# Kernel tuning notes

Hardware: AMD Instinct MI355X
Metric: run time of the kernel (lower is better)

The kernel has to match this reference:

```python
import jax, jax.numpy as jnp
import numpy as np
import math

B, N, E, H = 2, 10000, 160000, 128
ET = 8
EPS = 1e-5


def setup_inputs() -> dict:
    key = jax.random.key(0)
    ks = jax.random.split(key, 20)
    s = 1.0 / math.sqrt(H)
    inp = {
        "hidden": jax.random.normal(ks[0], (B, N, H), jnp.float32),
        "time_emb": jax.random.normal(ks[1], (B, N, H), jnp.float32),
        "edge_index": jax.random.randint(ks[2], (2, E), 0, N),
        "edge_type": jax.random.randint(ks[3], (E,), 0, ET),
        # parameters
        "edge_emb": jax.random.normal(ks[4], (ET, H), jnp.float32),
        "Wq": jax.random.normal(ks[5], (H, H), jnp.float32) * s,
        "bq": jnp.zeros((H,), jnp.float32),
        "Wk": jax.random.normal(ks[6], (H, H), jnp.float32) * s,
        "bk": jnp.zeros((H,), jnp.float32),
        "Wv": jax.random.normal(ks[7], (H, H), jnp.float32) * s,
        "bv": jnp.zeros((H,), jnp.float32),
        "We": jax.random.normal(ks[8], (H, 1), jnp.float32) * s,
        "be": jnp.zeros((1,), jnp.float32),
        "W1": jax.random.normal(ks[9], (3 * H, H), jnp.float32) * (1.0 / math.sqrt(3 * H)),
        "b1": jnp.zeros((H,), jnp.float32),
        "W2": jax.random.normal(ks[10], (H, H), jnp.float32) * s,
        "b2": jnp.zeros((H,), jnp.float32),
        "gamma": jnp.ones((H,), jnp.float32),
        "beta": jnp.zeros((H,), jnp.float32),
    }
    return inp


def _forward(hidden, time_emb, edge_index, edge_type, edge_emb,
             Wq, bq, Wk, bk, Wv, bv, We, be, W1, b1, W2, b2, gamma, beta):
    src, tgt = edge_index[0], edge_index[1]
    # edge-wise gathers: [B, E, H]
    src_h = hidden[:, src]
    tgt_h = hidden[:, tgt]
    src_t = time_emb[:, src]
    tgt_t = time_emb[:, tgt]
    edge_h = edge_emb[edge_type][None, :, :]  # [1, E, H] broadcasts over batch

    query = (tgt_h + tgt_t) @ Wq + bq
    key = (src_h + src_t + edge_h) @ Wk + bk
    value = (src_h + edge_h) @ Wv + bv

    logits = jnp.einsum("beh,beh->be", query, key) / math.sqrt(H)
    logits = logits + (edge_h @ We + be)[..., 0]  # edge bias broadcast over batch

    # segment softmax per target node (equivalent to the per-node masked softmax loop)
    lT = logits.T  # [E, B]
    seg_max = jax.ops.segment_max(lT, tgt, num_segments=N)          # [N, B]
    seg_max = jnp.where(jnp.isfinite(seg_max), seg_max, 0.0)
    ex = jnp.exp(lT - seg_max[tgt])                                  # [E, B]
    seg_sum = jax.ops.segment_sum(ex, tgt, num_segments=N)           # [N, B]
    weights = (ex / seg_sum[tgt]).T                                  # [B, E]

    messages = value * weights[..., None]                            # [B, E, H]
    # scatter-add to target nodes
    agg = jax.ops.segment_sum(jnp.swapaxes(messages, 0, 1), tgt, num_segments=N)  # [N, B, H]
    aggregated = jnp.swapaxes(agg, 0, 1)                             # [B, N, H]

    cat = jnp.concatenate([hidden, aggregated, time_emb], axis=-1)   # [B, N, 3H]
    updated = jax.nn.silu(cat @ W1 + b1) @ W2 + b2

    x = hidden + updated  # dropout p=0 -> identity
    mu = jnp.mean(x, axis=-1, keepdims=True)
    var = jnp.var(x, axis=-1, keepdims=True)
    return (x - mu) * jax.lax.rsqrt(var + EPS) * gamma + beta


def reference(hidden, time_emb, edge_index, edge_type, edge_emb,
              Wq, bq, Wk, bk, Wv, bv, We, be, W1, b1, W2, b2, gamma, beta):
    return _forward(hidden, time_emb, edge_index, edge_type, edge_emb,
                    Wq, bq, Wk, bk, Wv, bv, We, be, W1, b1, W2, b2, gamma, beta)
```

## Files before the change

kernel.cpp:

```cpp
#include <hip/hip_runtime.h>
#include <math.h>

constexpr int B_  = 2;
constexpr int N_  = 10000;
constexpr int E_  = 160000;
constexpr int H_  = 128;
constexpr int ET_ = 8;
constexpr float EPS_ = 1e-5f;
constexpr float RSQH = 0.08838834764831845f;

typedef __bf16 bf16x8 __attribute__((ext_vector_type(8)));
typedef short  short8 __attribute__((ext_vector_type(8)));
typedef float  f32x4  __attribute__((ext_vector_type(4)));
typedef unsigned short u16;

__device__ inline u16 bf16b(float f) {
    return __builtin_bit_cast(u16, (__bf16)f);
}

__device__ inline bf16x8 ldfrag(const u16* __restrict__ W, int kc, int nt, int lane) {
    short8 s = *(const short8*)(W + ((kc * 8 + nt) * 64 + lane) * 8);
    return __builtin_bit_cast(bf16x8, s);
}

__global__ __launch_bounds__(256)
void setup_kernel(const float* __restrict__ W1, const float* __restrict__ W2,
                  const float* __restrict__ Wq, const float* __restrict__ Wk,
                  const float* __restrict__ Wv,
                  u16* __restrict__ W1s, u16* __restrict__ W2s,
                  u16* __restrict__ Wqs, u16* __restrict__ Wks, u16* __restrict__ Wvs,
                  const float* __restrict__ edge_emb,
                  const float* __restrict__ bk, const float* __restrict__ bv,
                  const float* __restrict__ We, const float* __restrict__ be,
                  float* __restrict__ Kt, float* __restrict__ Vt, float* __restrict__ eb,
                  const int* __restrict__ tgt, int* __restrict__ hist)
{
    const int bid = blockIdx.x, tid = threadIdx.x;
    if (bid < 56) {
        int unit = bid >> 1, half = bid & 1;
        const float* src; u16* dst; int kc;
        if (unit < 12)      { src = W1; dst = W1s; kc = unit; }
        else if (unit < 16) { src = W2; dst = W2s; kc = unit - 12; }
        else if (unit < 20) { src = Wq; dst = Wqs; kc = unit - 16; }
        else if (unit < 24) { src = Wk; dst = Wks; kc = unit - 20; }
        else                { src = Wv; dst = Wvs; kc = unit - 24; }
        int nt = half * 4 + (tid >> 6), lane = tid & 63;
        int q = lane >> 4, c = lane & 15;
        int kbase = kc * 32 + q * 8;
        int col = nt * 16 + c;
        u16* out = dst + ((kc * 8 + nt) * 64 + lane) * 8;
#pragma unroll
        for (int j = 0; j < 8; ++j)
            out[j] = bf16b(src[(kbase + j) * H_ + col]);
    } else if (bid < 64) {
        int t = bid - 56;
        const float* ep = edge_emb + t * H_;
        __shared__ float red[2];
        int j = tid;
        if (j < 128) {
            float ak = bk[j], av = bv[j];
            for (int d = 0; d < H_; d += 4) {
                float e0 = ep[d], e1 = ep[d+1], e2 = ep[d+2], e3 = ep[d+3];
                ak += e0*Wk[(d+0)*H_+j] + e1*Wk[(d+1)*H_+j] + e2*Wk[(d+2)*H_+j] + e3*Wk[(d+3)*H_+j];
                av += e0*Wv[(d+0)*H_+j] + e1*Wv[(d+1)*H_+j] + e2*Wv[(d+2)*H_+j] + e3*Wv[(d+3)*H_+j];
            }
            Kt[t*H_ + j] = ak;
            Vt[t*H_ + j] = av;
            float pe = ep[j] * We[j];
#pragma unroll
            for (int off = 32; off; off >>= 1) pe += __shfl_xor(pe, off);
            if ((j & 63) == 0) red[j >> 6] = pe;
        }
        __syncthreads();
        if (j == 0) eb[t] = red[0] + red[1] + be[0];
    } else {
        int e = (bid - 64) * 256 + tid;
        if (e < E_) atomicAdd(&hist[tgt[e]], 1);
    }
}

__global__ __launch_bounds__(1024)
void scan_kernel(const int* __restrict__ hist, int* __restrict__ offs,
                 int* __restrict__ cursor)
{
    __shared__ int winc[16];
    const int tid = threadIdx.x, wave = tid >> 6, lane = tid & 63;
    int v[10];
    const int idx0 = tid * 10;
    int tot = 0;
#pragma unroll
    for (int i = 0; i < 10; ++i) {
        int idx = idx0 + i;
        v[i] = (idx < N_) ? hist[idx] : 0;
        tot += v[i];
    }
    int s = tot;
#pragma unroll
    for (int off = 1; off < 64; off <<= 1) {
        int t = __shfl_up(s, off);
        if (lane >= off) s += t;
    }
    if (lane == 63) winc[wave] = s;
    __syncthreads();
    if (tid < 16) {
        int si = winc[tid];
#pragma unroll
        for (int off = 1; off < 16; off <<= 1) {
            int t = __shfl_up(si, off);
            if (tid >= off) si += t;
        }
        winc[tid] = si;
    }
    __syncthreads();
    int wbase = (wave == 0) ? 0 : winc[wave - 1];
    int run = wbase + (s - tot);
#pragma unroll
    for (int i = 0; i < 10; ++i) {
        int idx = idx0 + i;
        if (idx < N_) { offs[idx] = run; cursor[idx] = run; }
        run += v[i];
    }
    if (tid == 0) offs[N_] = winc[15];
}

__global__ __launch_bounds__(256)
void scatter_qkv_kernel(const int* __restrict__ src, const int* __restrict__ tgt,
                        const int* __restrict__ type, int* __restrict__ cursor,
                        int* __restrict__ sorted,
                        const float* __restrict__ hidden, const float* __restrict__ time_emb,
                        const u16* __restrict__ Wqs, const u16* __restrict__ Wks,
                        const u16* __restrict__ Wvs, const float* __restrict__ bq,
                        u16* __restrict__ Q, u16* __restrict__ K, u16* __restrict__ V)
{
    if (blockIdx.x < 625) {
        int e = blockIdx.x * 256 + threadIdx.x;
        if (e < E_) {
            int t = tgt[e];
            int pos = atomicAdd(&cursor[t], 1);
            sorted[pos] = src[e] | (type[e] << 16);
        }
        return;
    }
    const int wv = threadIdx.x >> 6, lane = threadIdx.x & 63;
    const int tile = (blockIdx.x - 625) * 4 + wv;
    if (tile >= (B_ * N_) / 16) return;
    const int nbase = tile * 16;
    const int m = lane & 15, q = lane >> 4;
    const int koff = q * 8;

    bf16x8 aq[4], av[4];
    const float* hp = hidden   + (nbase + m) * H_ + koff;
    const float* tp = time_emb + (nbase + m) * H_ + koff;
#pragma unroll
    for (int kc = 0; kc < 4; ++kc) {
        float4 h0 = *(const float4*)(hp + kc * 32);
        float4 h1 = *(const float4*)(hp + kc * 32 + 4);
        float4 t0 = *(const float4*)(tp + kc * 32);
        float4 t1 = *(const float4*)(tp + kc * 32 + 4);
        bf16x8 fv, fq;
        fv[0]=(__bf16)h0.x; fv[1]=(__bf16)h0.y; fv[2]=(__bf16)h0.z; fv[3]=(__bf16)h0.w;
        fv[4]=(__bf16)h1.x; fv[5]=(__bf16)h1.y; fv[6]=(__bf16)h1.z; fv[7]=(__bf16)h1.w;
        fq[0]=(__bf16)(h0.x+t0.x); fq[1]=(__bf16)(h0.y+t0.y);
        fq[2]=(__bf16)(h0.z+t0.z); fq[3]=(__bf16)(h0.w+t0.w);
        fq[4]=(__bf16)(h1.x+t1.x); fq[5]=(__bf16)(h1.y+t1.y);
        fq[6]=(__bf16)(h1.z+t1.z); fq[7]=(__bf16)(h1.w+t1.w);
        av[kc] = fv; aq[kc] = fq;
    }

    f32x4 accq[8], acck[8], accv[8];
#pragma unroll
    for (int nt = 0; nt < 8; ++nt) { accq[nt] = (f32x4)0.f; acck[nt] = (f32x4)0.f; accv[nt] = (f32x4)0.f; }

#pragma unroll
    for (int kc = 0; kc < 4; ++kc) {
#pragma unroll
        for (int nt = 0; nt < 8; ++nt) {
            bf16x8 bfq = ldfrag(Wqs, kc, nt, lane);
            bf16x8 bfk = ldfrag(Wks, kc, nt, lane);
            bf16x8 bfv = ldfrag(Wvs, kc, nt, lane);
            accq[nt] = __builtin_amdgcn_mfma_f32_16x16x32_bf16(aq[kc], bfq, accq[nt], 0, 0, 0);
            acck[nt] = __builtin_amdgcn_mfma_f32_16x16x32_bf16(aq[kc], bfk, acck[nt], 0, 0, 0);
            accv[nt] = __builtin_amdgcn_mfma_f32_16x16x32_bf16(av[kc], bfv, accv[nt], 0, 0, 0);
        }
    }

#pragma unroll
    for (int nt = 0; nt < 8; ++nt) {
        int col = nt * 16 + m;
        float bqc = bq[col];
#pragma unroll
        for (int r = 0; r < 4; ++r) {
            int node = nbase + q * 4 + r;
            Q[node * H_ + col] = bf16b(accq[nt][r] + bqc);
            K[node * H_ + col] = bf16b(acck[nt][r]);
            V[node * H_ + col] = bf16b(accv[nt][r]);
        }
    }
}

__global__ __launch_bounds__(256)
void attn_kernel(const u16* __restrict__ Qb, const u16* __restrict__ Kb,
                 const u16* __restrict__ Vb,
                 const float* __restrict__ Kt, const float* __restrict__ Vt,
                 const float* __restrict__ eb,
                 const int* __restrict__ offs, const int* __restrict__ sorted,
                 u16* __restrict__ aggb)
{
    __shared__ float logit_s[4][64];
    __shared__ float bias_s[4][8];
    __shared__ int   pk_s[4][64];
    __shared__ __align__(16) u16 vt_s[8][128];

    const int tid = threadIdx.x;
    const int wv = tid >> 6, lane = tid & 63;
    const int g = lane >> 4, lam = lane & 15;

    for (int idx = tid; idx < ET_ * H_; idx += 256)
        vt_s[idx >> 7][idx & 127] = bf16b(Vt[idx]);
    __syncthreads();

    const int b = blockIdx.x & 1;
    const int n = (blockIdx.x >> 1) * 4 + wv;
    const int bn = b * N_ + n;
    const int beg = offs[n], end = offs[n + 1];
    const int bbase = b * N_;

    float q[8];
    {
        short8 s8 = *(const short8*)(Qb + (size_t)bn * H_ + lam * 8);
        bf16x8 qa = __builtin_bit_cast(bf16x8, s8);
#pragma unroll
        for (int j = 0; j < 8; ++j) q[j] = (float)qa[j];
    }

    {
        const float* k0p = Kt + (2 * g) * H_ + lam * 8;
        const float* k1p = Kt + (2 * g + 1) * H_ + lam * 8;
        float p0 = 0.f, p1 = 0.f;
#pragma unroll
        for (int j = 0; j < 8; ++j) { p0 += q[j] * k0p[j]; p1 += q[j] * k1p[j]; }
#pragma unroll
        for (int msk = 1; msk < 16; msk <<= 1) {
            p0 += __shfl_xor(p0, msk);
            p1 += __shfl_xor(p1, msk);
        }
        if (lam == 0) {
            bias_s[wv][2 * g]     = p0 * RSQH + eb[2 * g];
            bias_s[wv][2 * g + 1] = p1 * RSQH + eb[2 * g + 1];
        }
    }

    float m_run = -INFINITY, l = 0.f;
    float acc[8];
#pragma unroll
    for (int j = 0; j < 8; ++j) acc[j] = 0.f;

    for (int cb = beg; cb < end; cb += 64) {
        const int cnt = min(64, end - cb);
        pk_s[wv][lane] = (cb + lane < end) ? sorted[cb + lane] : 0;

        float gmax = -INFINITY;
        int c = g;
        for (; c + 4 < cnt; c += 8) {
            int pk0 = pk_s[wv][c];
            int pk1 = pk_s[wv][c + 4];
            int s0 = pk0 & 0xFFFF, t0 = pk0 >> 16;
            int s1 = pk1 & 0xFFFF, t1 = pk1 >> 16;
            short8 k80 = *(const short8*)(Kb + (size_t)(bbase + s0) * H_ + lam * 8);
            short8 k81 = *(const short8*)(Kb + (size_t)(bbase + s1) * H_ + lam * 8);
            bf16x8 ka0 = __builtin_bit_cast(bf16x8, k80);
            bf16x8 ka1 = __builtin_bit_cast(bf16x8, k81);
            float p0 = 0.f, p1 = 0.f;
#pragma unroll
            for (int j = 0; j < 8; ++j) {
                p0 += q[j] * (float)ka0[j];
                p1 += q[j] * (float)ka1[j];
            }
#pragma unroll
            for (int msk = 1; msk < 16; msk <<= 1) {
                p0 += __shfl_xor(p0, msk);
                p1 += __shfl_xor(p1, msk);
            }
            float lg0 = p0 * RSQH + bias_s[wv][t0];
            float lg1 = p1 * RSQH + bias_s[wv][t1];
            if (lam == 0) { logit_s[wv][c] = lg0; logit_s[wv][c + 4] = lg1; }
            gmax = fmaxf(gmax, fmaxf(lg0, lg1));
        }
        if (c < cnt) {
            int pk0 = pk_s[wv][c];
            int s0 = pk0 & 0xFFFF, t0 = pk0 >> 16;
            short8 k80 = *(const short8*)(Kb + (size_t)(bbase + s0) * H_ + lam * 8);
            bf16x8 ka0 = __builtin_bit_cast(bf16x8, k80);
            float p0 = 0.f;
#pragma unroll
            for (int j = 0; j < 8; ++j) p0 += q[j] * (float)ka0[j];
#pragma unroll
            for (int msk = 1; msk < 16; msk <<= 1) p0 += __shfl_xor(p0, msk);
            float lg0 = p0 * RSQH + bias_s[wv][t0];
            if (lam == 0) logit_s[wv][c] = lg0;
            gmax = fmaxf(gmax, lg0);
        }
        gmax = fmaxf(gmax, __shfl_xor(gmax, 16));
        gmax = fmaxf(gmax, __shfl_xor(gmax, 32));
        float Mn = fmaxf(m_run, gmax);
        float rs = __expf(m_run - Mn);
        l *= rs;
#pragma unroll
        for (int j = 0; j < 8; ++j) acc[j] *= rs;
        m_run = Mn;

        c = g;
        for (; c + 4 < cnt; c += 8) {
            int pk0 = pk_s[wv][c];
            int pk1 = pk_s[wv][c + 4];
            int s0 = pk0 & 0xFFFF, t0 = pk0 >> 16;
            int s1 = pk1 & 0xFFFF, t1 = pk1 >> 16;
            short8 v80  = *(const short8*)(Vb + (size_t)(bbase + s0) * H_ + lam * 8);
            short8 v81  = *(const short8*)(Vb + (size_t)(bbase + s1) * H_ + lam * 8);
            short8 vt80 = *(const short8*)(&vt_s[t0][lam * 8]);
            short8 vt81 = *(const short8*)(&vt_s[t1][lam * 8]);
            float w0 = __expf(logit_s[wv][c] - Mn);
            float w1 = __expf(logit_s[wv][c + 4] - Mn);
            l += w0 + w1;
            bf16x8 va0  = __builtin_bit_cast(bf16x8, v80);
            bf16x8 va1  = __builtin_bit_cast(bf16x8, v81);
            bf16x8 vta0 = __builtin_bit_cast(bf16x8, vt80);
            bf16x8 vta1 = __builtin_bit_cast(bf16x8, vt81);
#pragma unroll
            for (int j = 0; j < 8; ++j)
                acc[j] += w0 * ((float)va0[j] + (float)vta0[j])
                        + w1 * ((float)va1[j] + (float)vta1[j]);
        }
        if (c < cnt) {
            int pk0 = pk_s[wv][c];
            int s0 = pk0 & 0xFFFF, t0 = pk0 >> 16;
            short8 v80  = *(const short8*)(Vb + (size_t)(bbase + s0) * H_ + lam * 8);
            short8 vt80 = *(const short8*)(&vt_s[t0][lam * 8]);
            float w0 = __expf(logit_s[wv][c] - Mn);
            l += w0;
            bf16x8 va0  = __builtin_bit_cast(bf16x8, v80);
            bf16x8 vta0 = __builtin_bit_cast(bf16x8, vt80);
#pragma unroll
            for (int j = 0; j < 8; ++j)
                acc[j] += w0 * ((float)va0[j] + (float)vta0[j]);
        }
    }

#pragma unroll
    for (int j = 0; j < 8; ++j) {
        acc[j] += __shfl_xor(acc[j], 16);
        acc[j] += __shfl_xor(acc[j], 32);
    }
    l += __shfl_xor(l, 16);
    l += __shfl_xor(l, 32);

    if (g == 0) {
        float invL = (end > beg) ? 1.f / l : 0.f;
        bf16x8 o;
#pragma unroll
        for (int j = 0; j < 8; ++j) o[j] = (__bf16)(acc[j] * invL);
        *(short8*)(aggb + (size_t)bn * H_ + lam * 8) = __builtin_bit_cast(short8, o);
    }
}

__global__ __launch_bounds__(256)
void mlp_mfma_kernel(const float* __restrict__ hidden, const u16* __restrict__ aggb,
                     const float* __restrict__ time_emb,
                     const u16* __restrict__ W1s, const u16* __restrict__ W2s,
                     const float* __restrict__ b1, const float* __restrict__ b2,
                     const float* __restrict__ gamma, const float* __restrict__ beta,
                     float* __restrict__ out)
{
    __shared__ __align__(16) u16 h1s[4][16][136];
    const int wv = threadIdx.x >> 6, lane = threadIdx.x & 63;
    const int tile = blockIdx.x * 4 + wv;
    if (tile >= (B_ * N_) / 16) return;
    const int nbase = tile * 16;
    const int m = lane & 15, q = lane >> 4;
    const int koff = q * 8;

    bf16x8 a[12];
    const float* hp = hidden   + (nbase + m) * H_ + koff;
    const float* tp = time_emb + (nbase + m) * H_ + koff;
    const u16*   ap = aggb + (size_t)(nbase + m) * H_ + koff;
#pragma unroll
    for (int kc = 0; kc < 4; ++kc) {
        float4 h0 = *(const float4*)(hp + kc * 32);
        float4 h1 = *(const float4*)(hp + kc * 32 + 4);
        float4 t0 = *(const float4*)(tp + kc * 32);
        float4 t1 = *(const float4*)(tp + kc * 32 + 4);
        bf16x8 fh, ft;
        fh[0]=(__bf16)h0.x; fh[1]=(__bf16)h0.y; fh[2]=(__bf16)h0.z; fh[3]=(__bf16)h0.w;
        fh[4]=(__bf16)h1.x; fh[5]=(__bf16)h1.y; fh[6]=(__bf16)h1.z; fh[7]=(__bf16)h1.w;
        ft[0]=(__bf16)t0.x; ft[1]=(__bf16)t0.y; ft[2]=(__bf16)t0.z; ft[3]=(__bf16)t0.w;
        ft[4]=(__bf16)t1.x; ft[5]=(__bf16)t1.y; ft[6]=(__bf16)t1.z; ft[7]=(__bf16)t1.w;
        a[0 * 4 + kc] = fh;
        a[2 * 4 + kc] = ft;
        short8 s8 = *(const short8*)(ap + kc * 32);
        a[1 * 4 + kc] = __builtin_bit_cast(bf16x8, s8);
    }

    f32x4 acc[8];
#pragma unroll
    for (int nt = 0; nt < 8; ++nt) acc[nt] = (f32x4)0.f;
#pragma unroll
    for (int kc = 0; kc < 12; ++kc) {
#pragma unroll
        for (int nt = 0; nt < 8; ++nt) {
            bf16x8 bf = ldfrag(W1s, kc, nt, lane);
            acc[nt] = __builtin_amdgcn_mfma_f32_16x16x32_bf16(a[kc], bf, acc[nt], 0, 0, 0);
        }
    }

#pragma unroll
    for (int nt = 0; nt < 8; ++nt) {
        int col = nt * 16 + m;
        float bb = b1[col];
#pragma unroll
        for (int r = 0; r < 4; ++r) {
            float v = acc[nt][r] + bb;
            float h = v / (1.f + __expf(-v));
            h1s[wv][q * 4 + r][col] = bf16b(h);
        }
    }

    f32x4 acc2[8];
#pragma unroll
    for (int nt = 0; nt < 8; ++nt) acc2[nt] = (f32x4)0.f;
#pragma unroll
    for (int kc = 0; kc < 4; ++kc) {
        short8 s8 = *(const short8*)&h1s[wv][m][kc * 32 + koff];
        bf16x8 a2 = __builtin_bit_cast(bf16x8, s8);
#pragma unroll
        for (int nt = 0; nt < 8; ++nt) {
            bf16x8 bf = ldfrag(W2s, kc, nt, lane);
            acc2[nt] = __builtin_amdgcn_mfma_f32_16x16x32_bf16(a2, bf, acc2[nt], 0, 0, 0);
        }
    }

    float x[8][4];
#pragma unroll
    for (int nt = 0; nt < 8; ++nt) {
        int col = nt * 16 + m;
        float bb = b2[col];
#pragma unroll
        for (int r = 0; r < 4; ++r) {
            int node = nbase + q * 4 + r;
            x[nt][r] = hidden[node * H_ + col] + acc2[nt][r] + bb;
        }
    }
#pragma unroll
    for (int r = 0; r < 4; ++r) {
        float s = 0.f, ss = 0.f;
#pragma unroll
        for (int nt = 0; nt < 8; ++nt) { s += x[nt][r]; ss += x[nt][r] * x[nt][r]; }
#pragma unroll
        for (int off = 1; off < 16; off <<= 1) {
            s  += __shfl_xor(s, off);
            ss += __shfl_xor(ss, off);
        }
        float mu  = s * (1.f / H_);
        float var = ss * (1.f / H_) - mu * mu;
        float rs  = rsqrtf(var + EPS_);
        int node = nbase + q * 4 + r;
#pragma unroll
        for (int nt = 0; nt < 8; ++nt) {
            int col = nt * 16 + m;
            out[node * H_ + col] = (x[nt][r] - mu) * rs * gamma[col] + beta[col];
        }
    }
}

extern "C" void kernel_launch(void* const* d_in, const int* in_sizes, int n_in,
                              void* d_out, int out_size, void* d_ws, size_t ws_size,
                              hipStream_t stream)
{
    const float* hidden   = (const float*)d_in[0];
    const float* time_emb = (const float*)d_in[1];
    const int*   eidx     = (const int*)d_in[2];
    const int*   etype    = (const int*)d_in[3];
    const float* edge_emb = (const float*)d_in[4];
    const float* Wq = (const float*)d_in[5];
    const float* bq = (const float*)d_in[6];
    const float* Wk = (const float*)d_in[7];
    const float* bk = (const float*)d_in[8];
    const float* Wv = (const float*)d_in[9];
    const float* bv = (const float*)d_in[10];
    const float* We = (const float*)d_in[11];
    const float* be = (const float*)d_in[12];
    const float* W1 = (const float*)d_in[13];
    const float* b1 = (const float*)d_in[14];
    const float* W2 = (const float*)d_in[15];
    const float* b2 = (const float*)d_in[16];
    const float* gamma = (const float*)d_in[17];
    const float* beta  = (const float*)d_in[18];
    float* out = (float*)d_out;

    constexpr int BNH = B_ * N_ * H_;
    u16* Qb   = (u16*)d_ws;
    u16* Kb   = Qb + BNH;
    u16* Vb   = Kb + BNH;
    u16* aggb = Vb + BNH;
    float* Kt  = (float*)(aggb + BNH);
    float* Vt  = Kt + ET_ * H_;
    float* ebt = Vt + ET_ * H_;
    int* hist   = (int*)(ebt + ET_);
    int* offs   = hist + N_;
    int* cursor = offs + (N_ + 1);
    int* sorted = cursor + N_;
    uintptr_t wp = (uintptr_t)(sorted + E_);
    wp = (wp + 15) & ~(uintptr_t)15;
    u16* W1s = (u16*)wp;
    u16* W2s = W1s + 384 * 128;
    u16* Wqs = W2s + 128 * 128;
    u16* Wks = Wqs + 128 * 128;
    u16* Wvs = Wks + 128 * 128;

    const int* esrc = eidx;
    const int* etgt = eidx + E_;

    hipMemsetAsync(hist, 0, N_ * sizeof(int), stream);

    setup_kernel<<<64 + (E_ + 255) / 256, 256, 0, stream>>>(
        W1, W2, Wq, Wk, Wv, W1s, W2s, Wqs, Wks, Wvs,
        edge_emb, bk, bv, We, be, Kt, Vt, ebt, etgt, hist);
    scan_kernel<<<1, 1024, 0, stream>>>(hist, offs, cursor);
    scatter_qkv_kernel<<<625 + 313, 256, 0, stream>>>(
        esrc, etgt, etype, cursor, sorted,
        hidden, time_emb, Wqs, Wks, Wvs, bq, Qb, Kb, Vb);
    attn_kernel<<<(B_ * N_) / 4, 256, 0, stream>>>(Qb, Kb, Vb, Kt, Vt, ebt, offs, sorted, aggb);
    mlp_mfma_kernel<<<313, 256, 0, stream>>>(hidden, aggb, time_emb, W1s, W2s, b1, b2, gamma, beta, out);
}
```

Before: 195.7 us.

## Single-pass per-group online softmax in attention; precompute edge-type bias in QKV kernel

The attention kernel drops its two-pass chunk structure (logits to shared memory, then a max, then a second pass over V) in favour of one pass. Each 16-lane group keeps its own running max and sum, and K and V loads are issued together. Groups are merged with shuffles at the end. The per-node edge-type bias (q·Kt) moves into the QKV projection kernel, computed from fp32 accumulators and stored as a B*N*8 table. This removes a shared-memory round trip and a second gather loop, at the cost of extra exp and rescale work per edge and more register pressure.

```diff
diff --git a/kernel.cpp b/kernel.cpp
--- a/kernel.cpp
+++ b/kernel.cpp
@@ -130,7 +130,9 @@
                         const float* __restrict__ hidden, const float* __restrict__ time_emb,
                         const u16* __restrict__ Wqs, const u16* __restrict__ Wks,
                         const u16* __restrict__ Wvs, const float* __restrict__ bq,
-                        u16* __restrict__ Q, u16* __restrict__ K, u16* __restrict__ V)
+                        const float* __restrict__ KtF, const float* __restrict__ ebt,
+                        u16* __restrict__ Q, u16* __restrict__ K, u16* __restrict__ V,
+                        float* __restrict__ biasT)
 {
     if (blockIdx.x < 625) {
         int e = blockIdx.x * 256 + threadIdx.x;
@@ -184,14 +186,35 @@
         }
     }
 
+    float bqv[8];
+#pragma unroll
+    for (int nt = 0; nt < 8; ++nt) bqv[nt] = bq[nt * 16 + m];
+
+#pragma unroll
+    for (int t = 0; t < ET_; ++t) {
+        float kt[8];
+#pragma unroll
+        for (int nt = 0; nt < 8; ++nt) kt[nt] = KtF[t * H_ + nt * 16 + m];
+        float ebv = ebt[t];
+#pragma unroll
+        for (int r = 0; r < 4; ++r) {
+            float s = 0.f;
+#pragma unroll
+            for (int nt = 0; nt < 8; ++nt) s += (accq[nt][r] + bqv[nt]) * kt[nt];
+#pragma unroll
+            for (int msk = 1; msk < 16; msk <<= 1) s += __shfl_xor(s, msk);
+            if (m == 0)
+                biasT[(nbase + q * 4 + r) * ET_ + t] = s * RSQH + ebv;
+        }
+    }
+
 #pragma unroll
     for (int nt = 0; nt < 8; ++nt) {
         int col = nt * 16 + m;
-        float bqc = bq[col];
 #pragma unroll
         for (int r = 0; r < 4; ++r) {
             int node = nbase + q * 4 + r;
-            Q[node * H_ + col] = bf16b(accq[nt][r] + bqc);
+            Q[node * H_ + col] = bf16b(accq[nt][r] + bqv[nt]);
             K[node * H_ + col] = bf16b(acck[nt][r]);
             V[node * H_ + col] = bf16b(accv[nt][r]);
         }
@@ -200,20 +223,18 @@
 
 __global__ __launch_bounds__(256)
 void attn_kernel(const u16* __restrict__ Qb, const u16* __restrict__ Kb,
-                 const u16* __restrict__ Vb,
-                 const float* __restrict__ Kt, const float* __restrict__ Vt,
-                 const float* __restrict__ eb,
+                 const u16* __restrict__ Vb, const float* __restrict__ Vt,
+                 const float* __restrict__ biasT,
                  const int* __restrict__ offs, const int* __restrict__ sorted,
                  u16* __restrict__ aggb)
 {
-    __shared__ float logit_s[4][64];
     __shared__ float bias_s[4][8];
     __shared__ int   pk_s[4][64];
     __shared__ __align__(16) u16 vt_s[8][128];
 
     const int tid = threadIdx.x;
     const int wv = tid >> 6, lane = tid & 63;
-    const int g = lane >> 4, lam = lane & 15;
+    const int g = lane >> 4, lam = lane & 63 & 15;
 
     for (int idx = tid; idx < ET_ * H_; idx += 256)
         vt_s[idx >> 7][idx & 127] = bf16b(Vt[idx]);
@@ -225,6 +246,8 @@
     const int beg = offs[n], end = offs[n + 1];
     const int bbase = b * N_;
 
+    if (lane < 8) bias_s[wv][lane] = biasT[bn * ET_ + lane];
+
     float q[8];
     {
         short8 s8 = *(const short8*)(Qb + (size_t)bn * H_ + lam * 8);
@@ -233,24 +256,7 @@
         for (int j = 0; j < 8; ++j) q[j] = (float)qa[j];
     }
 
-    {
-        const float* k0p = Kt + (2 * g) * H_ + lam * 8;
-        const float* k1p = Kt + (2 * g + 1) * H_ + lam * 8;
-        float p0 = 0.f, p1 = 0.f;
-#pragma unroll
-        for (int j = 0; j < 8; ++j) { p0 += q[j] * k0p[j]; p1 += q[j] * k1p[j]; }
-#pragma unroll
-        for (int msk = 1; msk < 16; msk <<= 1) {
-            p0 += __shfl_xor(p0, msk);
-            p1 += __shfl_xor(p1, msk);
-        }
-        if (lam == 0) {
-            bias_s[wv][2 * g]     = p0 * RSQH + eb[2 * g];
-            bias_s[wv][2 * g + 1] = p1 * RSQH + eb[2 * g + 1];
-        }
-    }
-
-    float m_run = -INFINITY, l = 0.f;
+    float m_g = -INFINITY, l_g = 0.f;
     float acc[8];
 #pragma unroll
     for (int j = 0; j < 8; ++j) acc[j] = 0.f;
@@ -259,7 +265,6 @@
         const int cnt = min(64, end - cb);
         pk_s[wv][lane] = (cb + lane < end) ? sorted[cb + lane] : 0;
 
-        float gmax = -INFINITY;
         int c = g;
         for (; c + 4 < cnt; c += 8) {
             int pk0 = pk_s[wv][c];
@@ -268,6 +273,10 @@
             int s1 = pk1 & 0xFFFF, t1 = pk1 >> 16;
             short8 k80 = *(const short8*)(Kb + (size_t)(bbase + s0) * H_ + lam * 8);
             short8 k81 = *(const short8*)(Kb + (size_t)(bbase + s1) * H_ + lam * 8);
+            short8 v80 = *(const short8*)(Vb + (size_t)(bbase + s0) * H_ + lam * 8);
+            short8 v81 = *(const short8*)(Vb + (size_t)(bbase + s1) * H_ + lam * 8);
+            short8 vt80 = *(const short8*)(&vt_s[t0][lam * 8]);
+            short8 vt81 = *(const short8*)(&vt_s[t1][lam * 8]);
             bf16x8 ka0 = __builtin_bit_cast(bf16x8, k80);
             bf16x8 ka1 = __builtin_bit_cast(bf16x8, k81);
             float p0 = 0.f, p1 = 0.f;
@@ -283,13 +292,27 @@
             }
             float lg0 = p0 * RSQH + bias_s[wv][t0];
             float lg1 = p1 * RSQH + bias_s[wv][t1];
-            if (lam == 0) { logit_s[wv][c] = lg0; logit_s[wv][c + 4] = lg1; }
-            gmax = fmaxf(gmax, fmaxf(lg0, lg1));
+            float nm = fmaxf(m_g, fmaxf(lg0, lg1));
+            float sc = __expf(m_g - nm);
+            float w0 = __expf(lg0 - nm);
+            float w1 = __expf(lg1 - nm);
+            l_g = l_g * sc + w0 + w1;
+            bf16x8 va0  = __builtin_bit_cast(bf16x8, v80);
+            bf16x8 va1  = __builtin_bit_cast(bf16x8, v81);
+            bf16x8 vta0 = __builtin_bit_cast(bf16x8, vt80);
+            bf16x8 vta1 = __builtin_bit_cast(bf16x8, vt81);
+#pragma unroll
+            for (int j = 0; j < 8; ++j)
+                acc[j] = acc[j] * sc + w0 * ((float)va0[j] + (float)vta0[j])
+                                     + w1 * ((float)va1[j] + (float)vta1[j]);
+            m_g = nm;
         }
         if (c < cnt) {
             int pk0 = pk_s[wv][c];
             int s0 = pk0 & 0xFFFF, t0 = pk0 >> 16;
             short8 k80 = *(const short8*)(Kb + (size_t)(bbase + s0) * H_ + lam * 8);
+            short8 v80 = *(const short8*)(Vb + (size_t)(bbase + s0) * H_ + lam * 8);
+            short8 vt80 = *(const short8*)(&vt_s[t0][lam * 8]);
             bf16x8 ka0 = __builtin_bit_cast(bf16x8, k80);
             float p0 = 0.f;
 #pragma unroll
@@ -297,65 +320,35 @@
 #pragma unroll
             for (int msk = 1; msk < 16; msk <<= 1) p0 += __shfl_xor(p0, msk);
             float lg0 = p0 * RSQH + bias_s[wv][t0];
-            if (lam == 0) logit_s[wv][c] = lg0;
-            gmax = fmaxf(gmax, lg0);
-        }
-        gmax = fmaxf(gmax, __shfl_xor(gmax, 16));
-        gmax = fmaxf(gmax, __shfl_xor(gmax, 32));
-        float Mn = fmaxf(m_run, gmax);
-        float rs = __expf(m_run - Mn);
-        l *= rs;
-#pragma unroll
-        for (int j = 0; j < 8; ++j) acc[j] *= rs;
-        m_run = Mn;
-
-        c = g;
-        for (; c + 4 < cnt; c += 8) {
-            int pk0 = pk_s[wv][c];
-            int pk1 = pk_s[wv][c + 4];
-            int s0 = pk0 & 0xFFFF, t0 = pk0 >> 16;
-            int s1 = pk1 & 0xFFFF, t1 = pk1 >> 16;
-            short8 v80  = *(const short8*)(Vb + (size_t)(bbase + s0) * H_ + lam * 8);
-            short8 v81  = *(const short8*)(Vb + (size_t)(bbase + s1) * H_ + lam * 8);
-            short8 vt80 = *(const short8*)(&vt_s[t0][lam * 8]);
-            short8 vt81 = *(const short8*)(&vt_s[t1][lam * 8]);
-            float w0 = __expf(logit_s[wv][c] - Mn);
-            float w1 = __expf(logit_s[wv][c + 4] - Mn);
-            l += w0 + w1;
-            bf16x8 va0  = __builtin_bit_cast(bf16x8, v80);
-            bf16x8 va1  = __builtin_bit_cast(bf16x8, v81);
-            bf16x8 vta0 = __builtin_bit_cast(bf16x8, vt80);
-            bf16x8 vta1 = __builtin_bit_cast(bf16x8, vt81);
-#pragma unroll
-            for (int j = 0; j < 8; ++j)
-                acc[j] += w0 * ((float)va0[j] + (float)vta0[j])
-                        + w1 * ((float)va1[j] + (float)vta1[j]);
-        }
-        if (c < cnt) {
-            int pk0 = pk_s[wv][c];
-            int s0 = pk0 & 0xFFFF, t0 = pk0 >> 16;
-            short8 v80  = *(const short8*)(Vb + (size_t)(bbase + s0) * H_ + lam * 8);
-            short8 vt80 = *(const short8*)(&vt_s[t0][lam * 8]);
-            float w0 = __expf(logit_s[wv][c] - Mn);
-            l += w0;
+            float nm = fmaxf(m_g, lg0);
+            float sc = __expf(m_g - nm);
+            float w0 = __expf(lg0 - nm);
+            l_g = l_g * sc + w0;
             bf16x8 va0  = __builtin_bit_cast(bf16x8, v80);
             bf16x8 vta0 = __builtin_bit_cast(bf16x8, vt80);
 #pragma unroll
             for (int j = 0; j < 8; ++j)
-                acc[j] += w0 * ((float)va0[j] + (float)vta0[j]);
-        }
-    }
-
+                acc[j] = acc[j] * sc + w0 * ((float)va0[j] + (float)vta0[j]);
+            m_g = nm;
+        }
+    }
+
+    float M = fmaxf(m_g, __shfl_xor(m_g, 16));
+    M = fmaxf(M, __shfl_xor(M, 32));
+    float sc = (l_g > 0.f) ? __expf(m_g - M) : 0.f;
+    float lw = l_g * sc;
+    lw += __shfl_xor(lw, 16);
+    lw += __shfl_xor(lw, 32);
 #pragma unroll
     for (int j = 0; j < 8; ++j) {
-        acc[j] += __shfl_xor(acc[j], 16);
-        acc[j] += __shfl_xor(acc[j], 32);
-    }
-    l += __shfl_xor(l, 16);
-    l += __shfl_xor(l, 32);
+        float a = acc[j] * sc;
+        a += __shfl_xor(a, 16);
+        a += __shfl_xor(a, 32);
+        acc[j] = a;
+    }
 
     if (g == 0) {
-        float invL = (end > beg) ? 1.f / l : 0.f;
+        float invL = (end > beg) ? 1.f / lw : 0.f;
         bf16x8 o;
 #pragma unroll
         for (int j = 0; j < 8; ++j) o[j] = (__bf16)(acc[j] * invL);
@@ -504,7 +497,8 @@
     float* Kt  = (float*)(aggb + BNH);
     float* Vt  = Kt + ET_ * H_;
     float* ebt = Vt + ET_ * H_;
-    int* hist   = (int*)(ebt + ET_);
+    float* biasT = ebt + ET_;
+    int* hist   = (int*)(biasT + B_ * N_ * ET_);
     int* offs   = hist + N_;
     int* cursor = offs + (N_ + 1);
     int* sorted = cursor + N_;
@@ -527,7 +521,7 @@
     scan_kernel<<<1, 1024, 0, stream>>>(hist, offs, cursor);
     scatter_qkv_kernel<<<625 + 313, 256, 0, stream>>>(
         esrc, etgt, etype, cursor, sorted,
-        hidden, time_emb, Wqs, Wks, Wvs, bq, Qb, Kb, Vb);
-    attn_kernel<<<(B_ * N_) / 4, 256, 0, stream>>>(Qb, Kb, Vb, Kt, Vt, ebt, offs, sorted, aggb);
+        hidden, time_emb, Wqs, Wks, Wvs, bq, Kt, ebt, Qb, Kb, Vb, biasT);
+    attn_kernel<<<(B_ * N_) / 4, 256, 0, stream>>>(Qb, Kb, Vb, Vt, biasT, offs, sorted, aggb);
     mlp_mfma_kernel<<<313, 256, 0, stream>>>(hidden, aggb, time_emb, W1s, W2s, b1, b2, gamma, beta, out);
 }
```

New measurement: 196.9 us. About the same (+0.6%).
